# Optimization experiments

Hardware: AMD Instinct MI355X
Metric: run time of the kernel (lower is better)

Reference implementation:

```python
import jax, jax.numpy as jnp
import numpy as np

H = 4          # num attention heads
C1 = 64        # channel_num[0]
C2 = 128       # channel_num[1]
KV = C1 + C2   # 192
MLP = C1 * 4   # expand_ratio=4


def _layernorm(x, g, b, eps=1e-6):
    m = jnp.mean(x, axis=-1, keepdims=True)
    v = jnp.mean((x - m) ** 2, axis=-1, keepdims=True)
    return (x - m) * jax.lax.rsqrt(v + eps) * g + b


def setup_inputs() -> dict:
    key = jax.random.key(0)
    ks = jax.random.split(key, 12)
    B, N = 8, 3136
    s_q = 1.0 / np.sqrt(C1)
    s_kv = 1.0 / np.sqrt(KV)
    return {
        "emb1": jax.random.normal(ks[0], (B, N, C1), jnp.float32),
        "emb2": jax.random.normal(ks[1], (B, N, C2), jnp.float32),
        # per-head projection weights (nn.Linear convention: y = x @ W.T)
        "Wq": jax.random.uniform(ks[2], (H, C1, C1), jnp.float32, -s_q, s_q),
        "Wk": jax.random.uniform(ks[3], (H, KV, KV), jnp.float32, -s_kv, s_kv),
        "Wv": jax.random.uniform(ks[4], (H, KV, KV), jnp.float32, -s_kv, s_kv),
        "Wout": jax.random.uniform(ks[5], (C1, C1), jnp.float32, -s_q, s_q),
        "ln1_g": jnp.ones((C1,), jnp.float32),
        "ln1_b": jnp.zeros((C1,), jnp.float32),
        "lnall_g": jnp.ones((KV,), jnp.float32),
        "lnall_b": jnp.zeros((KV,), jnp.float32),
        "ffn_g": jnp.ones((C1,), jnp.float32),
        "ffn_b": jnp.zeros((C1,), jnp.float32),
        "fc1_w": jax.random.uniform(ks[6], (MLP, C1), jnp.float32, -s_q, s_q),
        "fc1_b": jnp.zeros((MLP,), jnp.float32),
        "fc2_w": jax.random.uniform(ks[7], (C1, MLP), jnp.float32, -1.0 / np.sqrt(MLP), 1.0 / np.sqrt(MLP)),
        "fc2_b": jnp.zeros((C1,), jnp.float32),
    }


def reference(emb1, emb2, Wq, Wk, Wv, Wout, ln1_g, ln1_b, lnall_g, lnall_b,
              ffn_g, ffn_b, fc1_w, fc1_b, fc2_w, fc2_b):
    # emb1: [B,N,C1], emb2: [B,N,C2]
    emb_all = jnp.concatenate([emb1, emb2], axis=2)          # [B,N,KV]
    cx1 = _layernorm(emb1, ln1_g, ln1_b)                     # [B,N,C1]
    ea = _layernorm(emb_all, lnall_g, lnall_b)               # [B,N,KV]

    # batched per-head projections (replaces Python loop over ModuleList)
    qT = jnp.einsum('bnc,hdc->bhdn', cx1, Wq)                # [B,H,C1,N]
    k = jnp.einsum('bnk,hdk->bhnd', ea, Wk)                  # [B,H,N,KV]
    vT = jnp.einsum('bnk,hdk->bhdn', ea, Wv)                 # [B,H,KV,N]

    scores = jnp.einsum('bhcn,bhnk->bhck', qT, k) / np.sqrt(KV)  # [B,H,C1,KV]
    # InstanceNorm2d over spatial dims (C1, KV) per (batch, head), affine=False
    m = jnp.mean(scores, axis=(2, 3), keepdims=True)
    v = jnp.mean((scores - m) ** 2, axis=(2, 3), keepdims=True)
    scores = (scores - m) * jax.lax.rsqrt(v + 1e-5)
    probs = jax.nn.softmax(scores, axis=3)                   # softmax over KV

    ctx = jnp.einsum('bhck,bhkn->bhcn', probs, vT)           # [B,H,C1,N]
    ctx = jnp.mean(ctx, axis=1).transpose(0, 2, 1)           # mean over heads -> [B,N,C1]
    o = ctx @ Wout.T                                         # [B,N,C1]

    cx = emb1 + o                                            # residual
    x = _layernorm(cx, ffn_g, ffn_b)
    x = jax.nn.gelu(x @ fc1_w.T + fc1_b, approximate=False)
    x = x @ fc2_w.T + fc2_b
    return x + cx
```

## Files before the change

### kernel.cpp

```cpp
#include <hip/hip_runtime.h>
#include <hip/hip_bf16.h>

typedef __hip_bfloat16 bf;
typedef unsigned short ushort_t;
typedef __attribute__((ext_vector_type(8))) short short8;
typedef __attribute__((ext_vector_type(4))) float f32x4;

#define NB 8
#define SEQ 3136
#define HD 4

__device__ __forceinline__ float lo_bf(unsigned u){ return __uint_as_float(u << 16); }
__device__ __forceinline__ float hi_bf(unsigned u){ return __uint_as_float(u & 0xffff0000u); }
__device__ __forceinline__ float b16f(ushort_t s){ return __uint_as_float(((unsigned)s) << 16); }
__device__ __forceinline__ unsigned short f2bfbits(float f){
  unsigned u = __float_as_uint(f);
  unsigned r = u + 0x7fffu + ((u >> 16) & 1u);
  return (unsigned short)(r >> 16);
}
__device__ __forceinline__ float ldin(const void* p, long i, bool isbf){
  return isbf ? __bfloat162float(((const bf*)p)[i]) : ((const float*)p)[i];
}
__device__ __forceinline__ float4 ld4(const void* p, long i, bool isbf){
  if (isbf){
    uint2 u = *reinterpret_cast<const uint2*>((const unsigned short*)p + i);
    return make_float4(lo_bf(u.x), hi_bf(u.x), lo_bf(u.y), hi_bf(u.y));
  }
  const float* f = (const float*)p + i;
  return make_float4(f[0], f[1], f[2], f[3]);
}
__device__ __forceinline__ ushort_t cvt1(const void* p, long i, bool isbf){
  return isbf ? ((const ushort_t*)p)[i] : f2bfbits(((const float*)p)[i]);
}
#define DTYPE_FLAG(p) (((const unsigned*)(p))[0] == 0x3F803F80u)

__device__ __forceinline__ float wsum(float v){
  #pragma unroll
  for (int o = 32; o > 0; o >>= 1) v += __shfl_xor(v, o, 64);
  return v;
}
__device__ __forceinline__ float wmax(float v){
  #pragma unroll
  for (int o = 32; o > 0; o >>= 1) v = fmaxf(v, __shfl_xor(v, o, 64));
  return v;
}

__global__ __launch_bounds__(256) void k_g(
    const void* __restrict__ emb1, const void* __restrict__ emb2,
    const void* __restrict__ g1, const void* __restrict__ b1,
    const void* __restrict__ ga, const void* __restrict__ ba,
    const void* __restrict__ Wq, const void* __restrict__ Wk, const void* __restrict__ Wv,
    const void* __restrict__ f1w, const void* __restrict__ f2w,
    ushort_t* __restrict__ part, ushort_t* __restrict__ eag,
    ushort_t* __restrict__ Wqb, ushort_t* __restrict__ Wkb, ushort_t* __restrict__ WvTb,
    ushort_t* __restrict__ f1wb, ushort_t* __restrict__ f2wb){
  bool isbf = DTYPE_FLAG(g1);
  int tid = threadIdx.x;
  int b = blockIdx.y, ch = blockIdx.x;
  if (ch >= 49){
    if (b != 0) return;
    int g = (ch - 49)*256 + tid;
    const int STR = 24*256;
    for (int i = g; i < 16384; i += STR) Wqb[i] = cvt1(Wq, i, isbf);
    for (int i = g; i < 147456; i += STR) Wkb[i] = cvt1(Wk, i, isbf);
    for (int i = g; i < 147456; i += STR){
      int hh = i / 36864, r = i - hh*36864;
      int j = r / 192, e = r - j*192;
      WvTb[i] = cvt1(Wv, (long)hh*36864 + e*192 + j, isbf);
    }
    for (int i = g; i < 16384; i += STR) f1wb[i] = cvt1(f1w, i, isbf);
    for (int i = g; i < 16384; i += STR) f2wb[i] = cvt1(f2w, i, isbf);
    return;
  }
  __shared__ __align__(16) ushort_t z1t[64*72];
  __shared__ __align__(16) ushort_t zat[192*72];
  int wave = tid >> 6, lane = tid & 63;
  int quad = lane >> 4, nl = lane & 15;
  long t0 = (long)b*SEQ + ch*64;
  float g1l = ldin(g1,lane,isbf), b1l = ldin(b1,lane,isbf);
  float ga0 = ldin(ga,lane,isbf),     ba0 = ldin(ba,lane,isbf);
  float ga1 = ldin(ga,64+lane,isbf),  ba1 = ldin(ba,64+lane,isbf);
  float ga2 = ldin(ga,128+lane,isbf), ba2 = ldin(ba,128+lane,isbf);
  #pragma unroll 4
  for (int k = 0; k < 16; ++k){
    int tok = wave*16 + k;
    long t = t0 + tok;
    float e1  = ldin(emb1, t*64 + lane, isbf);
    float e2a = ldin(emb2, t*128 + lane, isbf);
    float e2b = ldin(emb2, t*128 + 64 + lane, isbf);
    float s1 = wsum(e1), ss1 = wsum(e1*e1);
    float m1 = s1*(1.f/64.f);
    float r1 = rsqrtf(fmaxf(ss1*(1.f/64.f) - m1*m1, 0.f) + 1e-6f);
    z1t[lane*72 + tok] = f2bfbits((e1 - m1)*r1*g1l + b1l);
    float s23 = wsum(e2a+e2b), ss23 = wsum(e2a*e2a + e2b*e2b);
    float ma = (s1+s23)*(1.f/192.f);
    float ra = rsqrtf(fmaxf((ss1+ss23)*(1.f/192.f) - ma*ma, 0.f) + 1e-6f);
    unsigned short za0 = f2bfbits((e1  - ma)*ra*ga0 + ba0);
    unsigned short za1 = f2bfbits((e2a - ma)*ra*ga1 + ba1);
    unsigned short za2 = f2bfbits((e2b - ma)*ra*ga2 + ba2);
    zat[lane*72 + tok]       = za0;
    zat[(64+lane)*72 + tok]  = za1;
    zat[(128+lane)*72 + tok] = za2;
    eag[t*192 + lane]       = za0;
    eag[t*192 + 64 + lane]  = za1;
    eag[t*192 + 128 + lane] = za2;
  }
  __syncthreads();
  short8 a0 = *reinterpret_cast<const short8*>(&z1t[(wave*16+nl)*72 + quad*8]);
  short8 a1 = *reinterpret_cast<const short8*>(&z1t[(wave*16+nl)*72 + 32 + quad*8]);
  ushort_t* P = part + ((long)b*49 + ch)*12288;
  #pragma unroll
  for (int nt = 0; nt < 12; ++nt){
    f32x4 cd = {0.f,0.f,0.f,0.f};
    short8 b0 = *reinterpret_cast<const short8*>(&zat[(nt*16+nl)*72 + quad*8]);
    cd = __builtin_amdgcn_mfma_f32_16x16x32_bf16(a0, b0, cd, 0, 0, 0);
    short8 b1v = *reinterpret_cast<const short8*>(&zat[(nt*16+nl)*72 + 32 + quad*8]);
    cd = __builtin_amdgcn_mfma_f32_16x16x32_bf16(a1, b1v, cd, 0, 0, 0);
    #pragma unroll
    for (int reg = 0; reg < 4; ++reg)
      P[(wave*16 + quad*4 + reg)*192 + nt*16 + nl] = f2bfbits(cd[reg]);
  }
}

__global__ __launch_bounds__(64) void k_red(
    const ushort_t* __restrict__ part, ushort_t* __restrict__ Gb){
  int idx4 = blockIdx.x*64 + threadIdx.x;
  int b = idx4 / 3072, e4 = idx4 - b*3072;
  const ushort_t* p = part + (long)b*49*12288 + e4*4;
  float s0=0.f, s1=0.f, s2=0.f, s3=0.f;
  #pragma unroll
  for (int ch = 0; ch < 49; ++ch){
    uint2 u = *reinterpret_cast<const uint2*>(p + (long)ch*12288);
    s0 += lo_bf(u.x); s1 += hi_bf(u.x); s2 += lo_bf(u.y); s3 += hi_bf(u.y);
  }
  unsigned lo = (unsigned)f2bfbits(s0) | ((unsigned)f2bfbits(s1) << 16);
  unsigned hi = (unsigned)f2bfbits(s2) | ((unsigned)f2bfbits(s3) << 16);
  *reinterpret_cast<uint2*>(Gb + (long)idx4*4) = make_uint2(lo, hi);
}

__global__ __launch_bounds__(256) void k_att(
    const ushort_t* __restrict__ Gb, const ushort_t* __restrict__ Wqb,
    const ushort_t* __restrict__ Wkb, const ushort_t* __restrict__ WvTb,
    float* __restrict__ Mh){
  __shared__ __align__(16) ushort_t sT[192*72];
  __shared__ __align__(16) float    sS[64*196];
  __shared__ __align__(16) ushort_t sPh[64*200];
  __shared__ __align__(16) ushort_t sPl[64*200];
  __shared__ float red[8];
  __shared__ float stat[2];
  int h = blockIdx.x, b = blockIdx.y;
  int tid = threadIdx.x, wave = tid >> 6, lane = tid & 63;
  int quad = lane >> 4, nl = lane & 15;

  const ushort_t* Gp = Gb + (long)b*12288;
  short8 aG[6];
  #pragma unroll
  for (int ks = 0; ks < 6; ++ks)
    aG[ks] = *reinterpret_cast<const short8*>(Gp + (wave*16+nl)*192 + ks*32 + quad*8);
  const ushort_t* Wkp = Wkb + (long)h*36864;
  #pragma unroll
  for (int nt = 0; nt < 12; ++nt){
    f32x4 cd = {0.f,0.f,0.f,0.f};
    #pragma unroll
    for (int ks = 0; ks < 6; ++ks){
      short8 bw = *reinterpret_cast<const short8*>(Wkp + (nt*16+nl)*192 + ks*32 + quad*8);
      cd = __builtin_amdgcn_mfma_f32_16x16x32_bf16(aG[ks], bw, cd, 0, 0, 0);
    }
    #pragma unroll
    for (int reg = 0; reg < 4; ++reg)
      sT[(nt*16+nl)*72 + wave*16 + quad*4 + reg] = f2bfbits(cd[reg]);
  }
  __syncthreads();

  const ushort_t* Wqp = Wqb + (long)h*4096;
  short8 aQ[2];
  #pragma unroll
  for (int ks = 0; ks < 2; ++ks)
    aQ[ks] = *reinterpret_cast<const short8*>(Wqp + (wave*16+nl)*64 + ks*32 + quad*8);
  const float scale = 0.07216878364870323f;
  float ps = 0.f, pss = 0.f;
  #pragma unroll
  for (int nt = 0; nt < 12; ++nt){
    f32x4 cd = {0.f,0.f,0.f,0.f};
    #pragma unroll
    for (int ks = 0; ks < 2; ++ks){
      short8 bt = *reinterpret_cast<const short8*>(&sT[(nt*16+nl)*72 + ks*32 + quad*8]);
      cd = __builtin_amdgcn_mfma_f32_16x16x32_bf16(aQ[ks], bt, cd, 0, 0, 0);
    }
    #pragma unroll
    for (int reg = 0; reg < 4; ++reg){
      float v = cd[reg]*scale;
      sS[(wave*16 + quad*4 + reg)*196 + nt*16 + nl] = v;
      ps += v; pss += v*v;
    }
  }
  ps = wsum(ps); pss = wsum(pss);
  if (lane == 0){ red[wave] = ps; red[4+wave] = pss; }
  __syncthreads();
  if (tid == 0){
    float s  = red[0]+red[1]+red[2]+red[3];
    float s2 = red[4]+red[5]+red[6]+red[7];
    float m = s * (1.f/12288.f);
    stat[0] = m;
    stat[1] = rsqrtf(fmaxf(s2*(1.f/12288.f) - m*m, 0.f) + 1e-5f);
  }
  __syncthreads();
  float m = stat[0], r = stat[1];
  #pragma unroll 2
  for (int rr = 0; rr < 16; ++rr){
    int row = wave*16 + rr;
    float v0 = (sS[row*196+lane]     - m)*r;
    float v1 = (sS[row*196+64+lane]  - m)*r;
    float v2 = (sS[row*196+128+lane] - m)*r;
    float mx = wmax(fmaxf(v0, fmaxf(v1, v2)));
    float e0 = __expf(v0-mx), e1 = __expf(v1-mx), e2 = __expf(v2-mx);
    float inv = 1.f / wsum(e0+e1+e2);
    e0 *= inv; e1 *= inv; e2 *= inv;
    ushort_t h0 = f2bfbits(e0), h1 = f2bfbits(e1), h2 = f2bfbits(e2);
    sPh[row*200+lane]     = h0;  sPl[row*200+lane]     = f2bfbits(e0 - b16f(h0));
    sPh[row*200+64+lane]  = h1;  sPl[row*200+64+lane]  = f2bfbits(e1 - b16f(h1));
    sPh[row*200+128+lane] = h2;  sPl[row*200+128+lane] = f2bfbits(e2 - b16f(h2));
  }
  __syncthreads();

  short8 aPh[6], aPl[6];
  #pragma unroll
  for (int ks = 0; ks < 6; ++ks){
    aPh[ks] = *reinterpret_cast<const short8*>(&sPh[(wave*16+nl)*200 + ks*32 + quad*8]);
    aPl[ks] = *reinterpret_cast<const short8*>(&sPl[(wave*16+nl)*200 + ks*32 + quad*8]);
  }
  const ushort_t* Wvp = WvTb + (long)h*36864;
  float* Mb = Mh + ((long)b*HD + h)*12288;
  #pragma unroll
  for (int nt = 0; nt < 12; ++nt){
    f32x4 cd = {0.f,0.f,0.f,0.f};
    #pragma unroll
    for (int ks = 0; ks < 6; ++ks){
      short8 bw = *reinterpret_cast<const short8*>(Wvp + (nt*16+nl)*192 + ks*32 + quad*8);
      cd = __builtin_amdgcn_mfma_f32_16x16x32_bf16(aPl[ks], bw, cd, 0, 0, 0);
      cd = __builtin_amdgcn_mfma_f32_16x16x32_bf16(aPh[ks], bw, cd, 0, 0, 0);
    }
    #pragma unroll
    for (int reg = 0; reg < 4; ++reg)
      Mb[(wave*16 + quad*4 + reg)*192 + nt*16 + nl] = cd[reg];
  }
}

__global__ __launch_bounds__(256) void k_w2(
    const float* __restrict__ Mh, const void* __restrict__ Wout,
    const void* __restrict__ lng, ushort_t* __restrict__ W2){
  bool isbf = DTYPE_FLAG(lng);
  __shared__ __align__(16) float sM[64*49];
  int jc = blockIdx.x, b = blockIdx.y;
  int tid = threadIdx.x;
  for (int idx = tid; idx < 3072; idx += 256){
    int c = idx/48, j = idx - c*48;
    long base = (long)b*HD*12288 + c*192 + jc*48 + j;
    float s = Mh[base] + Mh[base+12288] + Mh[base+2*12288] + Mh[base+3*12288];
    sM[c*49 + j] = 0.25f*s;
  }
  __syncthreads();
  int ty = tid >> 4, tx = tid & 15;
  float acc[4][3];
  #pragma unroll
  for (int i=0;i<4;++i) for (int q=0;q<3;++q) acc[i][q]=0.f;
  for (int c = 0; c < 64; c += 4){
    float4 w4[4];
    #pragma unroll
    for (int i=0;i<4;++i) w4[i] = ld4(Wout, (long)(ty*4+i)*64 + c, isbf);
    float ww[4][4];
    #pragma unroll
    for (int i=0;i<4;++i){ ww[i][0]=w4[i].x; ww[i][1]=w4[i].y; ww[i][2]=w4[i].z; ww[i][3]=w4[i].w; }
    #pragma unroll
    for (int u = 0; u < 4; ++u){
      float t3[3];
      #pragma unroll
      for (int q=0;q<3;++q) t3[q] = sM[(c+u)*49 + tx*3 + q];
      #pragma unroll
      for (int i=0;i<4;++i)
        #pragma unroll
        for (int q=0;q<3;++q) acc[i][q] = fmaf(ww[i][u], t3[q], acc[i][q]);
    }
  }
  ushort_t* W2b = W2 + (long)b*12288;
  #pragma unroll
  for (int i=0;i<4;++i)
    #pragma unroll
    for (int q=0;q<3;++q)
      W2b[(ty*4+i)*192 + jc*48 + tx*3 + q] = f2bfbits(acc[i][q]);
}

__global__ __launch_bounds__(256) void k_tail(
    const void* __restrict__ emb1, const ushort_t* __restrict__ eag,
    const ushort_t* __restrict__ W2g,
    const void* __restrict__ ffg, const void* __restrict__ ffb,
    const ushort_t* __restrict__ f1wb, const void* __restrict__ f1b,
    const ushort_t* __restrict__ f2wb, const void* __restrict__ f2b,
    const void* __restrict__ lng, void* __restrict__ out){
  bool isbf = DTYPE_FLAG(lng);
  __shared__ __align__(16) ushort_t sCX[16*72];
  __shared__ __align__(16) ushort_t sX[16*88];
  __shared__ __align__(16) ushort_t sH[16*280];
  int tid = threadIdx.x, wave = tid >> 6, lane = tid & 63;
  int quad = lane >> 4, nl = lane & 15;
  int b = blockIdx.y;
  long tbase = (long)b*SEQ + blockIdx.x*16;

  short8 aO[6];
  #pragma unroll
  for (int kt = 0; kt < 6; ++kt)
    aO[kt] = *reinterpret_cast<const short8*>(eag + (tbase + nl)*192 + kt*32 + quad*8);
  const ushort_t* W2b = W2g + (long)b*12288;
  {
    f32x4 cd = {0.f,0.f,0.f,0.f};
    #pragma unroll
    for (int kt = 0; kt < 6; ++kt){
      short8 bf8 = *reinterpret_cast<const short8*>(W2b + (wave*16+nl)*192 + kt*32 + quad*8);
      cd = __builtin_amdgcn_mfma_f32_16x16x32_bf16(aO[kt], bf8, cd, 0, 0, 0);
    }
    #pragma unroll
    for (int reg = 0; reg < 4; ++reg){
      int tokl = quad*4 + reg;
      int chn = wave*16 + nl;
      float e1v = ldin(emb1, (tbase + tokl)*64 + chn, isbf);
      sCX[tokl*72 + chn] = f2bfbits(cd[reg] + e1v);
    }
  }
  __syncthreads();

  float gl = ldin(ffg, lane, isbf), bl = ldin(ffb, lane, isbf);
  #pragma unroll
  for (int k = 0; k < 4; ++k){
    int tokl = wave*4 + k;
    float c = b16f(sCX[tokl*72 + lane]);
    float s = wsum(c), ss = wsum(c*c);
    float m = s*(1.f/64.f);
    float r = rsqrtf(fmaxf(ss*(1.f/64.f) - m*m, 0.f) + 1e-6f);
    sX[tokl*88 + lane] = f2bfbits((c - m)*r*gl + bl);
  }
  __syncthreads();

  short8 aX[2];
  #pragma unroll
  for (int kt = 0; kt < 2; ++kt)
    aX[kt] = *reinterpret_cast<const short8*>(&sX[nl*88 + kt*32 + quad*8]);
  #pragma unroll
  for (int nn = 0; nn < 4; ++nn){
    int nt = wave*4 + nn;
    f32x4 cd = {0.f,0.f,0.f,0.f};
    #pragma unroll
    for (int kt = 0; kt < 2; ++kt){
      short8 bf8 = *reinterpret_cast<const short8*>(f1wb + (long)(nt*16+nl)*64 + kt*32 + quad*8);
      cd = __builtin_amdgcn_mfma_f32_16x16x32_bf16(aX[kt], bf8, cd, 0, 0, 0);
    }
    float bb = ldin(f1b, nt*16+nl, isbf);
    #pragma unroll
    for (int reg = 0; reg < 4; ++reg){
      float v = cd[reg] + bb;
      float h = 0.5f*v*(1.f + erff(v*0.70710678118654752f));
      sH[(quad*4 + reg)*280 + nt*16 + nl] = f2bfbits(h);
    }
  }
  __syncthreads();

  short8 aH[8];
  #pragma unroll
  for (int kt = 0; kt < 8; ++kt)
    aH[kt] = *reinterpret_cast<const short8*>(&sH[nl*280 + kt*32 + quad*8]);
  {
    f32x4 cd = {0.f,0.f,0.f,0.f};
    #pragma unroll
    for (int kt = 0; kt < 8; ++kt){
      short8 bf8 = *reinterpret_cast<const short8*>(f2wb + (long)(wave*16+nl)*256 + kt*32 + quad*8);
      cd = __builtin_amdgcn_mfma_f32_16x16x32_bf16(aH[kt], bf8, cd, 0, 0, 0);
    }
    float bb2 = ldin(f2b, wave*16+nl, isbf);
    #pragma unroll
    for (int reg = 0; reg < 4; ++reg){
      int tokl = quad*4 + reg;
      int chn = wave*16 + nl;
      float y = cd[reg] + bb2 + b16f(sCX[tokl*72 + chn]);
      if (isbf) sCX[tokl*72 + chn] = f2bfbits(y);
      else ((float*)out)[(tbase + tokl)*64 + chn] = y;
    }
  }
  if (isbf){
    __syncthreads();
    int tokl = wave*4 + (lane >> 4), prt = lane & 15;
    uint2 v = *reinterpret_cast<const uint2*>(&sCX[tokl*72 + prt*4]);
    *reinterpret_cast<uint2*>((ushort_t*)out + (tbase + tokl)*64 + prt*4) = v;
  }
}

extern "C" void kernel_launch(void* const* d_in, const int* in_sizes, int n_in,
                              void* d_out, int out_size, void* d_ws, size_t ws_size,
                              hipStream_t stream){
  const void* emb1 = d_in[0];
  const void* emb2 = d_in[1];
  const void* Wq   = d_in[2];
  const void* Wk   = d_in[3];
  const void* Wv   = d_in[4];
  const void* Wout = d_in[5];
  const void* ln1g = d_in[6];
  const void* ln1b = d_in[7];
  const void* lag  = d_in[8];
  const void* lab  = d_in[9];
  const void* ffg  = d_in[10];
  const void* ffb  = d_in[11];
  const void* f1w  = d_in[12];
  const void* f1b  = d_in[13];
  const void* f2w  = d_in[14];
  const void* f2b  = d_in[15];

  char* base = (char*)d_ws;
  ushort_t* part = (ushort_t*)base;
  ushort_t* ea   = (ushort_t*)(base + 9633792);
  ushort_t* Gb   = (ushort_t*)(base + 19267584);
  float*    Mh   = (float*)(base + 19464192);
  ushort_t* W2   = (ushort_t*)(base + 21037056);
  ushort_t* Wqb  = (ushort_t*)(base + 21233664);
  ushort_t* Wkb  = (ushort_t*)(base + 21266432);
  ushort_t* WvTb = (ushort_t*)(base + 21561344);
  ushort_t* f1wb = (ushort_t*)(base + 21856256);
  ushort_t* f2wb = (ushort_t*)(base + 21889024);

  k_g   <<<dim3(73,NB),   256, 0, stream>>>(emb1, emb2, ln1g, ln1b, lag, lab,
                                            Wq, Wk, Wv, f1w, f2w,
                                            part, ea, Wqb, Wkb, WvTb, f1wb, f2wb);
  k_red <<<384,            64, 0, stream>>>(part, Gb);
  k_att <<<dim3(HD,NB),   256, 0, stream>>>(Gb, Wqb, Wkb, WvTb, Mh);
  k_w2  <<<dim3(4,NB),    256, 0, stream>>>(Mh, Wout, ln1g, W2);
  k_tail<<<dim3(196,NB),  256, 0, stream>>>(emb1, ea, W2, ffg, ffb,
                                            f1wb, f1b, f2wb, f2b, ln1g, d_out);
}
```

Measured before the change: 183.4 us.

## Fuse partial reduction and Wout projection into attention kernel with last-block counter

Removes the separate k_red and k_w2 launches. Each attention block now sums the 49 per-chunk Gram partials for its batch straight into shared memory. The last of the four head blocks for a batch, found with an atomic counter and threadfence, averages Mh over the heads and runs the Wout projection with bf16 MFMA using a Wout copy pre-converted in k_g. This cuts launch overhead and intermediate buffers. In exchange, the four head blocks now redo the partial reduction, and that reduction runs on only 32 blocks instead of a wide grid.

```diff
diff --git a/kernel.cpp b/kernel.cpp
--- a/kernel.cpp
+++ b/kernel.cpp
@@ -21,14 +21,6 @@
 __device__ __forceinline__ float ldin(const void* p, long i, bool isbf){
   return isbf ? __bfloat162float(((const bf*)p)[i]) : ((const float*)p)[i];
 }
-__device__ __forceinline__ float4 ld4(const void* p, long i, bool isbf){
-  if (isbf){
-    uint2 u = *reinterpret_cast<const uint2*>((const unsigned short*)p + i);
-    return make_float4(lo_bf(u.x), hi_bf(u.x), lo_bf(u.y), hi_bf(u.y));
-  }
-  const float* f = (const float*)p + i;
-  return make_float4(f[0], f[1], f[2], f[3]);
-}
 __device__ __forceinline__ ushort_t cvt1(const void* p, long i, bool isbf){
   return isbf ? ((const ushort_t*)p)[i] : f2bfbits(((const float*)p)[i]);
 }
@@ -50,10 +42,11 @@
     const void* __restrict__ g1, const void* __restrict__ b1,
     const void* __restrict__ ga, const void* __restrict__ ba,
     const void* __restrict__ Wq, const void* __restrict__ Wk, const void* __restrict__ Wv,
-    const void* __restrict__ f1w, const void* __restrict__ f2w,
+    const void* __restrict__ f1w, const void* __restrict__ f2w, const void* __restrict__ Wout,
     ushort_t* __restrict__ part, ushort_t* __restrict__ eag,
     ushort_t* __restrict__ Wqb, ushort_t* __restrict__ Wkb, ushort_t* __restrict__ WvTb,
-    ushort_t* __restrict__ f1wb, ushort_t* __restrict__ f2wb){
+    ushort_t* __restrict__ f1wb, ushort_t* __restrict__ f2wb,
+    ushort_t* __restrict__ Woutb, unsigned* __restrict__ cnt){
   bool isbf = DTYPE_FLAG(g1);
   int tid = threadIdx.x;
   int b = blockIdx.y, ch = blockIdx.x;
@@ -61,7 +54,9 @@
     if (b != 0) return;
     int g = (ch - 49)*256 + tid;
     const int STR = 24*256;
+    if (g < 8) cnt[g] = 0;
     for (int i = g; i < 16384; i += STR) Wqb[i] = cvt1(Wq, i, isbf);
+    for (int i = g; i < 4096;  i += STR) Woutb[i] = cvt1(Wout, i, isbf);
     for (int i = g; i < 147456; i += STR) Wkb[i] = cvt1(Wk, i, isbf);
     for (int i = g; i < 147456; i += STR){
       int hh = i / 36864, r = i - hh*36864;
@@ -122,41 +117,40 @@
   }
 }
 
-__global__ __launch_bounds__(64) void k_red(
-    const ushort_t* __restrict__ part, ushort_t* __restrict__ Gb){
-  int idx4 = blockIdx.x*64 + threadIdx.x;
-  int b = idx4 / 3072, e4 = idx4 - b*3072;
-  const ushort_t* p = part + (long)b*49*12288 + e4*4;
-  float s0=0.f, s1=0.f, s2=0.f, s3=0.f;
-  #pragma unroll
-  for (int ch = 0; ch < 49; ++ch){
-    uint2 u = *reinterpret_cast<const uint2*>(p + (long)ch*12288);
-    s0 += lo_bf(u.x); s1 += hi_bf(u.x); s2 += lo_bf(u.y); s3 += hi_bf(u.y);
-  }
-  unsigned lo = (unsigned)f2bfbits(s0) | ((unsigned)f2bfbits(s1) << 16);
-  unsigned hi = (unsigned)f2bfbits(s2) | ((unsigned)f2bfbits(s3) << 16);
-  *reinterpret_cast<uint2*>(Gb + (long)idx4*4) = make_uint2(lo, hi);
-}
-
 __global__ __launch_bounds__(256) void k_att(
-    const ushort_t* __restrict__ Gb, const ushort_t* __restrict__ Wqb,
+    const ushort_t* __restrict__ part, const ushort_t* __restrict__ Wqb,
     const ushort_t* __restrict__ Wkb, const ushort_t* __restrict__ WvTb,
-    float* __restrict__ Mh){
+    const ushort_t* __restrict__ Woutb,
+    float* __restrict__ Mh, unsigned* __restrict__ cnt, ushort_t* __restrict__ W2){
   __shared__ __align__(16) ushort_t sT[192*72];
   __shared__ __align__(16) float    sS[64*196];
   __shared__ __align__(16) ushort_t sPh[64*200];
   __shared__ __align__(16) ushort_t sPl[64*200];
   __shared__ float red[8];
   __shared__ float stat[2];
+  __shared__ unsigned sOld;
   int h = blockIdx.x, b = blockIdx.y;
   int tid = threadIdx.x, wave = tid >> 6, lane = tid & 63;
   int quad = lane >> 4, nl = lane & 15;
 
-  const ushort_t* Gp = Gb + (long)b*12288;
+  const ushort_t* pb = part + (long)b*49*12288;
+  for (int g = tid; g < 3072; g += 256){
+    float a0=0.f, a1=0.f, a2=0.f, a3=0.f;
+    for (int ch = 0; ch < 49; ++ch){
+      uint2 u = *reinterpret_cast<const uint2*>(pb + (long)ch*12288 + g*4);
+      a0 += lo_bf(u.x); a1 += hi_bf(u.x); a2 += lo_bf(u.y); a3 += hi_bf(u.y);
+    }
+    int e = g*4; int c = e/192, j = e - c*192;
+    unsigned lo = (unsigned)f2bfbits(a0) | ((unsigned)f2bfbits(a1) << 16);
+    unsigned hi = (unsigned)f2bfbits(a2) | ((unsigned)f2bfbits(a3) << 16);
+    *reinterpret_cast<uint2*>(&sPh[c*200 + j]) = make_uint2(lo, hi);
+  }
+  __syncthreads();
+
   short8 aG[6];
   #pragma unroll
   for (int ks = 0; ks < 6; ++ks)
-    aG[ks] = *reinterpret_cast<const short8*>(Gp + (wave*16+nl)*192 + ks*32 + quad*8);
+    aG[ks] = *reinterpret_cast<const short8*>(&sPh[(wave*16+nl)*200 + ks*32 + quad*8]);
   const ushort_t* Wkp = Wkb + (long)h*36864;
   #pragma unroll
   for (int nt = 0; nt < 12; ++nt){
@@ -244,50 +238,43 @@
     for (int reg = 0; reg < 4; ++reg)
       Mb[(wave*16 + quad*4 + reg)*192 + nt*16 + nl] = cd[reg];
   }
-}
-
-__global__ __launch_bounds__(256) void k_w2(
-    const float* __restrict__ Mh, const void* __restrict__ Wout,
-    const void* __restrict__ lng, ushort_t* __restrict__ W2){
-  bool isbf = DTYPE_FLAG(lng);
-  __shared__ __align__(16) float sM[64*49];
-  int jc = blockIdx.x, b = blockIdx.y;
-  int tid = threadIdx.x;
-  for (int idx = tid; idx < 3072; idx += 256){
-    int c = idx/48, j = idx - c*48;
-    long base = (long)b*HD*12288 + c*192 + jc*48 + j;
-    float s = Mh[base] + Mh[base+12288] + Mh[base+2*12288] + Mh[base+3*12288];
-    sM[c*49 + j] = 0.25f*s;
-  }
-  __syncthreads();
-  int ty = tid >> 4, tx = tid & 15;
-  float acc[4][3];
-  #pragma unroll
-  for (int i=0;i<4;++i) for (int q=0;q<3;++q) acc[i][q]=0.f;
-  for (int c = 0; c < 64; c += 4){
-    float4 w4[4];
-    #pragma unroll
-    for (int i=0;i<4;++i) w4[i] = ld4(Wout, (long)(ty*4+i)*64 + c, isbf);
-    float ww[4][4];
-    #pragma unroll
-    for (int i=0;i<4;++i){ ww[i][0]=w4[i].x; ww[i][1]=w4[i].y; ww[i][2]=w4[i].z; ww[i][3]=w4[i].w; }
-    #pragma unroll
-    for (int u = 0; u < 4; ++u){
-      float t3[3];
+
+  __threadfence();
+  if (tid == 0) sOld = atomicAdd(&cnt[b], 1u);
+  __syncthreads();
+  if (sOld == 3u){
+    __threadfence();
+    const float* M0 = Mh + (long)b*HD*12288;
+    for (int g = tid; g < 3072; g += 256){
+      float4 x0 = ((const float4*)M0)[g];
+      float4 x1 = ((const float4*)(M0 + 12288))[g];
+      float4 x2 = ((const float4*)(M0 + 24576))[g];
+      float4 x3 = ((const float4*)(M0 + 36864))[g];
+      int e = g*4; int c = e/192, j = e - c*192;
+      sT[(j+0)*72 + c] = f2bfbits(0.25f*(x0.x+x1.x+x2.x+x3.x));
+      sT[(j+1)*72 + c] = f2bfbits(0.25f*(x0.y+x1.y+x2.y+x3.y));
+      sT[(j+2)*72 + c] = f2bfbits(0.25f*(x0.z+x1.z+x2.z+x3.z));
+      sT[(j+3)*72 + c] = f2bfbits(0.25f*(x0.w+x1.w+x2.w+x3.w));
+    }
+    __syncthreads();
+    short8 aW[2];
+    #pragma unroll
+    for (int ks = 0; ks < 2; ++ks)
+      aW[ks] = *reinterpret_cast<const short8*>(Woutb + (wave*16+nl)*64 + ks*32 + quad*8);
+    ushort_t* W2b = W2 + (long)b*12288;
+    #pragma unroll
+    for (int nt = 0; nt < 12; ++nt){
+      f32x4 cd = {0.f,0.f,0.f,0.f};
       #pragma unroll
-      for (int q=0;q<3;++q) t3[q] = sM[(c+u)*49 + tx*3 + q];
+      for (int ks = 0; ks < 2; ++ks){
+        short8 bm = *reinterpret_cast<const short8*>(&sT[(nt*16+nl)*72 + ks*32 + quad*8]);
+        cd = __builtin_amdgcn_mfma_f32_16x16x32_bf16(aW[ks], bm, cd, 0, 0, 0);
+      }
       #pragma unroll
-      for (int i=0;i<4;++i)
-        #pragma unroll
-        for (int q=0;q<3;++q) acc[i][q] = fmaf(ww[i][u], t3[q], acc[i][q]);
-    }
-  }
-  ushort_t* W2b = W2 + (long)b*12288;
-  #pragma unroll
-  for (int i=0;i<4;++i)
-    #pragma unroll
-    for (int q=0;q<3;++q)
-      W2b[(ty*4+i)*192 + jc*48 + tx*3 + q] = f2bfbits(acc[i][q]);
+      for (int reg = 0; reg < 4; ++reg)
+        W2b[(wave*16 + quad*4 + reg)*192 + nt*16 + nl] = f2bfbits(cd[reg]);
+    }
+  }
 }
 
 __global__ __launch_bounds__(256) void k_tail(
@@ -415,21 +402,21 @@
   char* base = (char*)d_ws;
   ushort_t* part = (ushort_t*)base;
   ushort_t* ea   = (ushort_t*)(base + 9633792);
-  ushort_t* Gb   = (ushort_t*)(base + 19267584);
-  float*    Mh   = (float*)(base + 19464192);
-  ushort_t* W2   = (ushort_t*)(base + 21037056);
-  ushort_t* Wqb  = (ushort_t*)(base + 21233664);
-  ushort_t* Wkb  = (ushort_t*)(base + 21266432);
-  ushort_t* WvTb = (ushort_t*)(base + 21561344);
-  ushort_t* f1wb = (ushort_t*)(base + 21856256);
-  ushort_t* f2wb = (ushort_t*)(base + 21889024);
+  float*    Mh   = (float*)(base + 19267584);
+  ushort_t* W2   = (ushort_t*)(base + 20840448);
+  ushort_t* Wqb  = (ushort_t*)(base + 21037056);
+  ushort_t* Wkb  = (ushort_t*)(base + 21069824);
+  ushort_t* WvTb = (ushort_t*)(base + 21364736);
+  ushort_t* f1wb = (ushort_t*)(base + 21659648);
+  ushort_t* f2wb = (ushort_t*)(base + 21692416);
+  ushort_t* Woutb= (ushort_t*)(base + 21725184);
+  unsigned* cnt  = (unsigned*)(base + 21733376);
 
   k_g   <<<dim3(73,NB),   256, 0, stream>>>(emb1, emb2, ln1g, ln1b, lag, lab,
-                                            Wq, Wk, Wv, f1w, f2w,
-                                            part, ea, Wqb, Wkb, WvTb, f1wb, f2wb);
-  k_red <<<384,            64, 0, stream>>>(part, Gb);
-  k_att <<<dim3(HD,NB),   256, 0, stream>>>(Gb, Wqb, Wkb, WvTb, Mh);
-  k_w2  <<<dim3(4,NB),    256, 0, stream>>>(Mh, Wout, ln1g, W2);
+                                            Wq, Wk, Wv, f1w, f2w, Wout,
+                                            part, ea, Wqb, Wkb, WvTb, f1wb, f2wb,
+                                            Woutb, cnt);
+  k_att <<<dim3(HD,NB),   256, 0, stream>>>(part, Wqb, Wkb, WvTb, Woutb, Mh, cnt, W2);
   k_tail<<<dim3(196,NB),  256, 0, stream>>>(emb1, ea, W2, ffg, ffb,
                                             f1wb, f1b, f2wb, f2b, ln1g, d_out);
 }
```

After: 215.8 us. +17.7%, slower.
